# Performance work log

Hardware: AMD Instinct MI355X
Metric: run time of the kernel (lower is better)

The kernel has to match this reference:

```python
import jax, jax.numpy as jnp
import numpy as np

N = 100000      # nodes
E = 3200000     # edges (avg degree 32)
F_IN = 128      # data.num_features
H = 64          # hidden_channels
L = 64          # num_layers
C = 47          # data.num_classes
ALPHA = 0.1
THETA = 0.5


def setup_inputs() -> dict:
    key = jax.random.key(0)
    ks = jax.random.split(key, 8)
    x = jax.random.normal(ks[0], (N, F_IN), dtype=jnp.float32)
    edge_index = jax.random.randint(ks[1], (2, E), 0, N, dtype=jnp.int64)
    # Linear(F_IN, H), Linear(H, C), and L shared GCN2Conv weights [H, H]
    W1 = jax.random.normal(ks[2], (F_IN, H), dtype=jnp.float32) * 0.05
    b1 = jnp.zeros((H,), dtype=jnp.float32)
    conv_W = jax.random.normal(ks[3], (L, H, H), dtype=jnp.float32) * 0.05
    W2 = jax.random.normal(ks[4], (H, C), dtype=jnp.float32) * 0.05
    b2 = jnp.zeros((C,), dtype=jnp.float32)
    return {"x": x, "edge_index": edge_index, "W1": W1, "b1": b1,
            "conv_W": conv_W, "W2": W2, "b2": b2}


def reference(x, edge_index, W1, b1, conv_W, W2, b2):
    # --- normalized adjacency with renormalization trick: D^-1/2 (A + I) D^-1/2, transposed ---
    sl = jnp.arange(N, dtype=edge_index.dtype)
    r = jnp.concatenate([edge_index[1], sl])  # adj_t rows (destinations)
    c = jnp.concatenate([edge_index[0], sl])  # adj_t cols (sources)
    deg = jax.ops.segment_sum(jnp.ones((r.shape[0],), jnp.float32), r, num_segments=N)
    dinv = jax.lax.rsqrt(deg)                 # self-loops guarantee deg >= 1
    w = dinv[r] * dinv[c]                     # [E + N] edge weights

    def spmm(h):  # A_hat @ h via gather + segment scatter-add
        return jax.ops.segment_sum(w[:, None] * h[c], r, num_segments=N)

    # dropout is identity in eval mode
    x0 = jax.nn.relu(x @ W1 + b1)             # [N, H]
    betas = jnp.log(THETA / jnp.arange(1, L + 1, dtype=jnp.float32) + 1.0)

    def step(h, layer):
        Wl, beta = layer
        p = spmm(h)
        s = (1.0 - ALPHA) * p + ALPHA * x0    # initial-residual mix
        h = jax.nn.relu((1.0 - beta) * s + beta * (s @ Wl))  # identity mapping
        return h, None

    h, _ = jax.lax.scan(step, x0, (conv_W, betas))
    logits = h @ W2 + b2                      # [N, C]
    return jax.nn.log_softmax(logits, axis=-1)
```

## Files before the change

kernel.cpp:

```cpp
#include <hip/hip_runtime.h>
#include <hip/hip_bf16.h>
#include <math.h>

#define NN 100000
#define NE 3200000
#define FIN 128
#define HD 64
#define NL 64
#define NC 47
#define RPW 4
#define WPB 4
#define RPB (RPW * WPB)

#define SEGSH 13
#define NSEG 13
#define NKEY (NN * NSEG)
#define KB ((NKEY + 1023) / 1024)


__device__ __forceinline__ float bf2f(unsigned short u) {
    union { unsigned int i; float f; } v; v.i = ((unsigned int)u) << 16; return v.f;
}
__device__ __forceinline__ unsigned short f2bf(float f) {
    __hip_bfloat16 h = __float2bfloat16(f);
    return *reinterpret_cast<unsigned short*>(&h);
}
__device__ __forceinline__ float bflo(unsigned int u) {
    union { unsigned int i; float f; } v; v.i = u << 16; return v.f;
}
__device__ __forceinline__ float bfhi(unsigned int u) {
    union { unsigned int i; float f; } v; v.i = u & 0xFFFF0000u; return v.f;
}
__device__ __forceinline__ float fin_at(const void* p, int isf32, size_t i) {
    return isf32 ? ((const float*)p)[i]
                 : __bfloat162float(((const __hip_bfloat16*)p)[i]);
}
__device__ __forceinline__ int edge_at(const void* p, int is64, size_t i) {
    return is64 ? (int)((const long long*)p)[i] : ((const int*)p)[i];
}

__device__ __forceinline__ unsigned int gpair(const unsigned short* __restrict__ g,
                                              int ca, int cb, int half, int moff) {
    int cc = half ? cb : ca;
    return *reinterpret_cast<const unsigned int*>(
        reinterpret_cast<const char*>(g) + (((size_t)cc) << 7) + moff);
}


__global__ void detect_kernel(const void* __restrict__ x, const void* __restrict__ eidx,
                              int* __restrict__ flags) {
    if (threadIdx.x == 0 && blockIdx.x == 0) {
        const unsigned short* u = (const unsigned short*)x;
        int sane = 0;
        for (int i = 0; i < 64; i++) {
            unsigned short v = u[2 * i];
            int e = (v >> 7) & 0xFF;
            if ((v & 0x7FFF) == 0 || (e >= 90 && e <= 141)) sane++;
        }
        flags[0] = (sane >= 48) ? 0 : 1;
        const int* e32 = (const int*)eidx;
        int nz = 0;
        for (int i = 0; i < 64; i++) if (e32[2 * i + 1] != 0) nz++;
        flags[1] = (nz == 0) ? 1 : 0;
    }
}


__global__ void key_count(const void* __restrict__ eidx, const int* __restrict__ flags,
                          int* __restrict__ cnt) {
    int e = blockIdx.x * blockDim.x + threadIdx.x;
    if (e < NE) {
        int is64 = flags[1];
        int s = edge_at(eidx, is64, (size_t)e);
        int d = edge_at(eidx, is64, (size_t)NE + e);
        atomicAdd(&cnt[d * NSEG + (s >> SEGSH)], 1);
    }
}

__global__ __launch_bounds__(1024) void scan_reduce(const int* __restrict__ cnt,
                                                    int* __restrict__ bsum) {
    __shared__ int lds[1024];
    int tid = threadIdx.x;
    int i = blockIdx.x * 1024 + tid;
    lds[tid] = (i < NKEY) ? cnt[i] : 0;
    __syncthreads();
    for (int off = 512; off > 0; off >>= 1) {
        if (tid < off) lds[tid] += lds[tid + off];
        __syncthreads();
    }
    if (tid == 0) bsum[blockIdx.x] = lds[0];
}

__global__ __launch_bounds__(1024) void scan_mid(int* __restrict__ bsum, int* __restrict__ total_out) {
    __shared__ int lds[1024];
    __shared__ int base_s;
    int tid = threadIdx.x;
    if (tid == 0) base_s = 0;
    __syncthreads();
    for (int chunk = 0; chunk < KB; chunk += 1024) {
        int i = chunk + tid;
        int v = (i < KB) ? bsum[i] : 0;
        lds[tid] = v;
        __syncthreads();
        for (int off = 1; off < 1024; off <<= 1) {
            int t = (tid >= off) ? lds[tid - off] : 0;
            __syncthreads();
            lds[tid] += t;
            __syncthreads();
        }
        int incl = lds[tid];
        int base = base_s;
        if (i < KB) bsum[i] = base + incl - v;
        __syncthreads();
        if (tid == 1023) base_s = base + incl;
        __syncthreads();
    }
    if (tid == 0) *total_out = base_s;
}

__global__ __launch_bounds__(1024) void scan_final(const int* __restrict__ cnt,
                                                   const int* __restrict__ bsum,
                                                   int* __restrict__ keyptr) {
    __shared__ int lds[1024];
    int tid = threadIdx.x;
    int i = blockIdx.x * 1024 + tid;
    int v = (i < NKEY) ? cnt[i] : 0;
    lds[tid] = v;
    __syncthreads();
    for (int off = 1; off < 1024; off <<= 1) {
        int t = (tid >= off) ? lds[tid - off] : 0;
        __syncthreads();
        lds[tid] += t;
        __syncthreads();
    }
    if (i < NKEY) keyptr[i] = bsum[blockIdx.x] + lds[tid] - v;
}

__global__ void dinv_kernel(const int* __restrict__ keyptr, float* __restrict__ dinv) {
    int i = blockIdx.x * blockDim.x + threadIdx.x;
    if (i < NN) {
        int deg = keyptr[(i + 1) * NSEG] - keyptr[i * NSEG];
        dinv[i] = rsqrtf(1.0f + (float)deg);
    }
}

__global__ void scatter_kernel(const void* __restrict__ eidx, const int* __restrict__ flags,
                               const int* __restrict__ keyptr, int* __restrict__ fill,
                               int* __restrict__ col) {
    int e = blockIdx.x * blockDim.x + threadIdx.x;
    if (e < NE) {
        int is64 = flags[1];
        int s = edge_at(eidx, is64, (size_t)e);
        int d = edge_at(eidx, is64, (size_t)NE + e);
        int key = d * NSEG + (s >> SEGSH);
        int pos = keyptr[key] + atomicAdd(&fill[key], 1);
        col[pos] = s;
    }
}


__global__ __launch_bounds__(256) void x0_kernel(const void* __restrict__ x,
                                                 const void* __restrict__ W1,
                                                 const void* __restrict__ b1,
                                                 const int* __restrict__ flags,
                                                 const float* __restrict__ dinv,
                                                 unsigned short* __restrict__ x0b,
                                                 unsigned short* __restrict__ g0) {
    __shared__ float lw[FIN * HD];
    int isf = flags[0];
    int tid = threadIdx.x;
    for (int i = tid; i < FIN * HD; i += 256) lw[i] = fin_at(W1, isf, i);
    __syncthreads();
    int wave = tid >> 6, lane = tid & 63;
    int row0 = blockIdx.x * RPB + wave * RPW;
    if (row0 >= NN) return;
    unsigned int pa01, pa23, pb01, pb23;
    {
        unsigned short a0 = f2bf(fin_at(x, isf, (size_t)(row0 + 0) * FIN + lane));
        unsigned short a1 = f2bf(fin_at(x, isf, (size_t)(row0 + 1) * FIN + lane));
        unsigned short a2 = f2bf(fin_at(x, isf, (size_t)(row0 + 2) * FIN + lane));
        unsigned short a3 = f2bf(fin_at(x, isf, (size_t)(row0 + 3) * FIN + lane));
        unsigned short c0 = f2bf(fin_at(x, isf, (size_t)(row0 + 0) * FIN + 64 + lane));
        unsigned short c1 = f2bf(fin_at(x, isf, (size_t)(row0 + 1) * FIN + 64 + lane));
        unsigned short c2 = f2bf(fin_at(x, isf, (size_t)(row0 + 2) * FIN + 64 + lane));
        unsigned short c3 = f2bf(fin_at(x, isf, (size_t)(row0 + 3) * FIN + 64 + lane));
        pa01 = ((unsigned int)a0 << 16) | a1;  pa23 = ((unsigned int)a2 << 16) | a3;
        pb01 = ((unsigned int)c0 << 16) | c1;  pb23 = ((unsigned int)c2 << 16) | c3;
    }
    float bias = fin_at(b1, isf, lane);
    float d0 = bias, d1 = bias, d2 = bias, d3 = bias;
    #pragma unroll 8
    for (int k = 0; k < 64; k++) {
        float w = lw[k * HD + lane];
        unsigned int b01 = __shfl(pa01, k, 64);
        unsigned int b23 = __shfl(pa23, k, 64);
        union { unsigned int i; float f; } f0, f1, f2, f3;
        f0.i = b01 & 0xFFFF0000u; f1.i = b01 << 16;
        f2.i = b23 & 0xFFFF0000u; f3.i = b23 << 16;
        d0 += f0.f * w; d1 += f1.f * w; d2 += f2.f * w; d3 += f3.f * w;
    }
    #pragma unroll 8
    for (int k = 0; k < 64; k++) {
        float w = lw[(64 + k) * HD + lane];
        unsigned int b01 = __shfl(pb01, k, 64);
        unsigned int b23 = __shfl(pb23, k, 64);
        union { unsigned int i; float f; } f0, f1, f2, f3;
        f0.i = b01 & 0xFFFF0000u; f1.i = b01 << 16;
        f2.i = b23 & 0xFFFF0000u; f3.i = b23 << 16;
        d0 += f0.f * w; d1 += f1.f * w; d2 += f2.f * w; d3 += f3.f * w;
    }
    float dd[RPW] = {d0, d1, d2, d3};
    #pragma unroll
    for (int r = 0; r < RPW; r++) {
        int row = row0 + r;
        if (row >= NN) continue;
        float v = fmaxf(dd[r], 0.0f);
        x0b[(size_t)row * HD + lane] = f2bf(v);
        g0[(size_t)row * HD + lane] = f2bf(dinv[row] * v);
    }
}


__global__ __launch_bounds__(256, 8) void layer_fused(const int* __restrict__ keyptr,
                                                      const int* __restrict__ col,
                                                      const float* __restrict__ dinv,
                                                      const unsigned short* __restrict__ g_in,
                                                      const unsigned short* __restrict__ x0b,
                                                      unsigned short* __restrict__ g_out,
                                                      const void* __restrict__ convW, int layer,
                                                      const int* __restrict__ flags, float beta) {
    __shared__ float lw[HD * HD];
    int isf = flags[0];
    size_t wbase = (size_t)layer * HD * HD;
    int tid = threadIdx.x;
    for (int i = tid; i < HD * HD; i += 256) lw[i] = fin_at(convW, isf, wbase + i);
    __syncthreads();

    int wave = __builtin_amdgcn_readfirstlane(tid >> 6);
    int lane = tid & 63;
    int half = lane >> 5;
    int moff = (lane & 31) << 2;

    int row0 = blockIdx.x * RPB + wave * RPW;

    float sacc[RPW];
    float dsc[RPW];
    #pragma unroll
    for (int r = 0; r < RPW; r++) {
        int row = row0 + r;
        if (row >= NN) { sacc[r] = 0.0f; dsc[r] = 1.0f; continue; }
        float a = bf2f(g_in[((size_t)row << 6) + lane]);
        float pe = 0.0f, po = 0.0f;
        int j = keyptr[row * NSEG];
        int end = keyptr[(row + 1) * NSEG];
        for (; j + 8 <= end; j += 8) {
            int c0 = col[j + 0], c1 = col[j + 1], c2 = col[j + 2], c3 = col[j + 3];
            int c4 = col[j + 4], c5 = col[j + 5], c6 = col[j + 6], c7 = col[j + 7];
            unsigned int u0 = gpair(g_in, c0, c1, half, moff);
            unsigned int u1 = gpair(g_in, c2, c3, half, moff);
            unsigned int u2 = gpair(g_in, c4, c5, half, moff);
            unsigned int u3 = gpair(g_in, c6, c7, half, moff);
            pe += bflo(u0); po += bfhi(u0);
            pe += bflo(u1); po += bfhi(u1);
            pe += bflo(u2); po += bfhi(u2);
            pe += bflo(u3); po += bfhi(u3);
        }
        for (; j + 2 <= end; j += 2) {
            unsigned int u = gpair(g_in, col[j], col[j + 1], half, moff);
            pe += bflo(u); po += bfhi(u);
        }
        for (; j < end; j++) {
            int c = col[j];
            a += bf2f(g_in[((size_t)c << 6) + lane]);
        }
        pe += __shfl_xor(pe, 32, 64);
        po += __shfl_xor(po, 32, 64);
        float ge = __shfl(pe, lane >> 1, 64);
        float go = __shfl(po, lane >> 1, 64);
        a += (lane & 1) ? go : ge;

        float di = dinv[row];
        dsc[r] = di;
        sacc[r] = 0.9f * (di * a) + 0.1f * bf2f(x0b[((size_t)row << 6) + lane]);
    }

    unsigned int p01 = ((unsigned int)f2bf(sacc[0]) << 16) | f2bf(sacc[1]);
    unsigned int p23 = ((unsigned int)f2bf(sacc[2]) << 16) | f2bf(sacc[3]);
    float d0 = 0.0f, d1 = 0.0f, d2 = 0.0f, d3 = 0.0f;
    #pragma unroll 8
    for (int k = 0; k < 64; k++) {
        float w = lw[k * HD + lane];
        unsigned int b01 = __shfl(p01, k, 64);
        unsigned int b23 = __shfl(p23, k, 64);
        union { unsigned int i; float f; } f0, f1, f2, f3;
        f0.i = b01 & 0xFFFF0000u; f1.i = b01 << 16;
        f2.i = b23 & 0xFFFF0000u; f3.i = b23 << 16;
        d0 += f0.f * w; d1 += f1.f * w;
        d2 += f2.f * w; d3 += f3.f * w;
    }

    float dd[RPW] = {d0, d1, d2, d3};
    float omb = 1.0f - beta;
    #pragma unroll
    for (int r = 0; r < RPW; r++) {
        int row = row0 + r;
        if (row >= NN) continue;
        float res = omb * sacc[r] + beta * dd[r];
        g_out[((size_t)row << 6) + lane] = f2bf(dsc[r] * fmaxf(res, 0.0f));
    }
}


__global__ __launch_bounds__(256) void out_kernel(const unsigned short* __restrict__ g,
                                                  const float* __restrict__ dinv,
                                                  const void* __restrict__ W2,
                                                  const void* __restrict__ b2,
                                                  const int* __restrict__ flags,
                                                  void* __restrict__ out) {
    __shared__ float lw[HD * 64];
    int isf = flags[0];
    int tid = threadIdx.x;
    for (int i = tid; i < HD * 64; i += 256) {
        int k = i >> 6, j = i & 63;
        lw[i] = (j < NC) ? fin_at(W2, isf, (size_t)k * NC + j) : 0.0f;
    }
    __syncthreads();
    int row = blockIdx.x * 4 + (tid >> 6);
    int lane = tid & 63;
    if (row >= NN) return;
    float hv = bf2f(g[(size_t)row * HD + lane]) / dinv[row];
    float acc = (lane < NC) ? fin_at(b2, isf, lane) : 0.0f;
    #pragma unroll 8
    for (int k = 0; k < 64; k++) {
        float hk = __shfl(hv, k, 64);
        acc += hk * lw[k * 64 + lane];
    }
    float mv = (lane < NC) ? acc : -1e30f;
    for (int off = 32; off > 0; off >>= 1) mv = fmaxf(mv, __shfl_xor(mv, off, 64));
    float ex = (lane < NC) ? expf(acc - mv) : 0.0f;
    float se = ex;
    for (int off = 32; off > 0; off >>= 1) se += __shfl_xor(se, off, 64);
    float res = acc - mv - logf(se);
    if (lane < NC) {
        size_t oi = (size_t)row * NC + lane;
        if (isf) ((float*)out)[oi] = res;
        else     ((__hip_bfloat16*)out)[oi] = __float2bfloat16(res);
    }
}


static inline size_t align256(size_t x) { return (x + 255) & ~(size_t)255; }

extern "C" void kernel_launch(void* const* d_in, const int* in_sizes, int n_in,
                              void* d_out, int out_size, void* d_ws, size_t ws_size,
                              hipStream_t stream) {
    const void* x     = d_in[0];
    const void* eidx  = d_in[1];
    const void* W1    = d_in[2];
    const void* b1    = d_in[3];
    const void* convW = d_in[4];
    const void* W2    = d_in[5];
    const void* b2    = d_in[6];

    char* p = (char*)d_ws;
    size_t off = 0;
    auto alloc = [&](size_t bytes) { void* r = p + off; off += align256(bytes); return r; };
    int*            flags   = (int*)alloc(256);
    int*            cnt     = (int*)alloc((size_t)NKEY * 4);
    int*            fill    = (int*)alloc((size_t)NKEY * 4);
    int*            keyptr  = (int*)alloc((size_t)(NKEY + 1) * 4);
    int*            bsum    = (int*)alloc((size_t)KB * 4);
    float*          dinv    = (float*)alloc((size_t)NN * 4);
    int*            col     = (int*)alloc((size_t)NE * 4);
    unsigned short* x0b     = (unsigned short*)alloc((size_t)NN * HD * 2);
    unsigned short* hA      = (unsigned short*)alloc((size_t)NN * HD * 2);
    unsigned short* hB      = (unsigned short*)alloc((size_t)NN * HD * 2);

    detect_kernel<<<1, 64, 0, stream>>>(x, eidx, flags);

    hipMemsetAsync(cnt, 0, (size_t)NKEY * 4, stream);
    hipMemsetAsync(fill, 0, (size_t)NKEY * 4, stream);
    key_count<<<(NE + 255) / 256, 256, 0, stream>>>(eidx, flags, cnt);
    scan_reduce<<<KB, 1024, 0, stream>>>(cnt, bsum);
    scan_mid<<<1, 1024, 0, stream>>>(bsum, keyptr + NKEY);
    scan_final<<<KB, 1024, 0, stream>>>(cnt, bsum, keyptr);
    dinv_kernel<<<(NN + 255) / 256, 256, 0, stream>>>(keyptr, dinv);
    scatter_kernel<<<(NE + 255) / 256, 256, 0, stream>>>(eidx, flags, keyptr, fill, col);

    int fb = (NN + RPB - 1) / RPB;
    x0_kernel<<<fb, 256, 0, stream>>>(x, W1, b1, flags, dinv, x0b, hA);

    unsigned short* gin = hA;
    unsigned short* gout = hB;
    for (int l = 0; l < NL; l++) {
        float beta = logf(0.5f / (float)(l + 1) + 1.0f);
        layer_fused<<<fb, 256, 0, stream>>>(keyptr, col, dinv, gin, x0b, gout,
                                            convW, l, flags, beta);
        unsigned short* t = gin; gin = gout; gout = t;
    }
    out_kernel<<<(NN + 3) / 4, 256, 0, stream>>>(gin, dinv, W2, b2, flags, (void*)d_out);
}
```

Measured before the change: 7.173 ms.

## Interleave neighbor gathers across rows by source segment for cache locality

The gather loop is restructured so each wave walks source-node segments in the outer loop and its four rows in the inner loop. All rows then touch the same source range of g_in at roughly the same time, which should improve L2 locality for the random gathers. The odd-edge tail is folded into the paired gather using a mask. The cost is more loop overhead, extra keyptr loads, and shorter inner loops per segment, which lowers memory-level parallelism.

```diff
diff --git a/kernel.cpp b/kernel.cpp
--- a/kernel.cpp
+++ b/kernel.cpp
@@ -240,8 +240,46 @@
     int lane = tid & 63;
     int half = lane >> 5;
     int moff = (lane & 31) << 2;
+    float mh = half ? 0.0f : 1.0f;
 
     int row0 = blockIdx.x * RPB + wave * RPW;
+
+    float pe[RPW], po[RPW];
+    int jc[RPW];
+    #pragma unroll
+    for (int r = 0; r < RPW; r++) {
+        pe[r] = 0.0f; po[r] = 0.0f;
+        int row = row0 + r;
+        jc[r] = (row < NN) ? keyptr[row * NSEG] : 0;
+    }
+
+    for (int seg = 0; seg < NSEG; seg++) {
+        #pragma unroll
+        for (int r = 0; r < RPW; r++) {
+            int row = row0 + r;
+            if (row >= NN) continue;
+            int j = jc[r];
+            int end = keyptr[row * NSEG + seg + 1];
+            jc[r] = end;
+            for (; j + 4 <= end; j += 4) {
+                int c0 = col[j + 0], c1 = col[j + 1];
+                int c2 = col[j + 2], c3 = col[j + 3];
+                unsigned int u0 = gpair(g_in, c0, c1, half, moff);
+                unsigned int u1 = gpair(g_in, c2, c3, half, moff);
+                pe[r] += bflo(u0); po[r] += bfhi(u0);
+                pe[r] += bflo(u1); po[r] += bfhi(u1);
+            }
+            for (; j + 2 <= end; j += 2) {
+                unsigned int u = gpair(g_in, col[j], col[j + 1], half, moff);
+                pe[r] += bflo(u); po[r] += bfhi(u);
+            }
+            if (j < end) {
+                int c = col[j];
+                unsigned int u = gpair(g_in, c, c, half, moff);
+                pe[r] += mh * bflo(u); po[r] += mh * bfhi(u);
+            }
+        }
+    }
 
     float sacc[RPW];
     float dsc[RPW];
@@ -249,36 +287,11 @@
     for (int r = 0; r < RPW; r++) {
         int row = row0 + r;
         if (row >= NN) { sacc[r] = 0.0f; dsc[r] = 1.0f; continue; }
-        float a = bf2f(g_in[((size_t)row << 6) + lane]);
-        float pe = 0.0f, po = 0.0f;
-        int j = keyptr[row * NSEG];
-        int end = keyptr[(row + 1) * NSEG];
-        for (; j + 8 <= end; j += 8) {
-            int c0 = col[j + 0], c1 = col[j + 1], c2 = col[j + 2], c3 = col[j + 3];
-            int c4 = col[j + 4], c5 = col[j + 5], c6 = col[j + 6], c7 = col[j + 7];
-            unsigned int u0 = gpair(g_in, c0, c1, half, moff);
-            unsigned int u1 = gpair(g_in, c2, c3, half, moff);
-            unsigned int u2 = gpair(g_in, c4, c5, half, moff);
-            unsigned int u3 = gpair(g_in, c6, c7, half, moff);
-            pe += bflo(u0); po += bfhi(u0);
-            pe += bflo(u1); po += bfhi(u1);
-            pe += bflo(u2); po += bfhi(u2);
-            pe += bflo(u3); po += bfhi(u3);
-        }
-        for (; j + 2 <= end; j += 2) {
-            unsigned int u = gpair(g_in, col[j], col[j + 1], half, moff);
-            pe += bflo(u); po += bfhi(u);
-        }
-        for (; j < end; j++) {
-            int c = col[j];
-            a += bf2f(g_in[((size_t)c << 6) + lane]);
-        }
-        pe += __shfl_xor(pe, 32, 64);
-        po += __shfl_xor(po, 32, 64);
-        float ge = __shfl(pe, lane >> 1, 64);
-        float go = __shfl(po, lane >> 1, 64);
-        a += (lane & 1) ? go : ge;
-
+        float p = pe[r] + __shfl_xor(pe[r], 32, 64);
+        float q = po[r] + __shfl_xor(po[r], 32, 64);
+        float ge = __shfl(p, lane >> 1, 64);
+        float go = __shfl(q, lane >> 1, 64);
+        float a = ((lane & 1) ? go : ge) + bf2f(g_in[((size_t)row << 6) + lane]);
         float di = dinv[row];
         dsc[r] = di;
         sacc[r] = 0.9f * (di * a) + 0.1f * bf2f(x0b[((size_t)row << 6) + lane]);
```

Result: slower. 12.30 ms (+71.5%).
